# Optimization experiments

Measured on AMD Instinct MI355X. Metric: run time of the kernel, lower is better.

Reference implementation:

```python
import jax, jax.numpy as jnp
import numpy as np

B, N, M = 2, 16200, 128
DIM, QK_DIM, HEADS, GS = 256, 256, 8, 128


def setup_inputs() -> dict:
    key = jax.random.key(0)
    ks = jax.random.split(key, 10)
    sorted_x = jax.random.normal(ks[0], (B, N, DIM), dtype=jnp.float32)
    prototypes = jax.random.normal(ks[1], (B, M, DIM), dtype=jnp.float32)
    # idx_last must be a per-batch permutation of 0..N-1 (scatter-back to original order)
    idx_last = jnp.argsort(jax.random.uniform(ks[2], (B, N)), axis=-1).astype(jnp.int32)[..., None]
    s = 0.02
    Wq = jax.random.normal(ks[3], (DIM, QK_DIM), dtype=jnp.float32) * s
    Wk = jax.random.normal(ks[4], (DIM, QK_DIM), dtype=jnp.float32) * s
    Wv = jax.random.normal(ks[5], (DIM, DIM), dtype=jnp.float32) * s
    Wpk = jax.random.normal(ks[6], (DIM, QK_DIM), dtype=jnp.float32) * s
    Wpv = jax.random.normal(ks[7], (DIM, DIM), dtype=jnp.float32) * s
    Wproj = jax.random.normal(ks[8], (DIM, DIM), dtype=jnp.float32) * s
    return {"sorted_x": sorted_x, "idx_last": idx_last, "prototypes": prototypes,
            "Wq": Wq, "Wk": Wk, "Wv": Wv, "Wpk": Wpk, "Wpv": Wpv, "Wproj": Wproj}


def _iasa(sorted_x, idx_last, prototypes, Wq, Wk, Wv, Wpk, Wpv, Wproj):
    b, n, dim = sorted_x.shape
    h = HEADS
    gs = min(n, GS)
    ng = (n + gs - 1) // gs
    pad_n = ng * gs - n
    dq = Wq.shape[1] // h   # qk head dim
    dv = Wv.shape[1] // h   # v head dim
    scale = 1.0 / jnp.sqrt(jnp.asarray(dq, sorted_x.dtype))

    q = sorted_x @ Wq
    k = sorted_x @ Wk
    v = sorted_x @ Wv

    # pad q with flipped tail (pad_n tokens) -> [b, ng*gs, qk]
    q_pad = jnp.concatenate([q, q[:, n - pad_n:n][:, ::-1]], axis=1)
    qh = q_pad.reshape(b, ng, gs, h, dq).transpose(0, 1, 3, 2, 4)  # b ng h gs d

    def windows(t, c):
        # pad with flipped last (pad_n + gs) tokens -> length (ng+1)*gs, then
        # overlapping windows of 2*gs with stride gs (== torch unfold)
        t_pad = jnp.concatenate([t, t[:, n - pad_n - gs:n][:, ::-1]], axis=1)
        tr = t_pad.reshape(b, ng + 1, gs, c)
        win = jnp.concatenate([tr[:, :-1], tr[:, 1:]], axis=2)  # b ng 2gs c
        return win.reshape(b, ng, 2 * gs, h, c // h).transpose(0, 1, 3, 2, 4)  # b ng h 2gs d

    kw = windows(k, Wk.shape[1])
    vw = windows(v, Wv.shape[1])

    # local overlapping-window attention
    a1 = jax.nn.softmax(jnp.einsum('bghqd,bghkd->bghqk', qh, kw) * scale, axis=-1)
    o1 = jnp.einsum('bghqk,bghkd->bghqd', a1, vw)

    # global prototype cross-attention
    kg = (prototypes @ Wpk).reshape(b, -1, h, dq).transpose(0, 2, 1, 3)  # b h m d
    vg = (prototypes @ Wpv).reshape(b, -1, h, dv).transpose(0, 2, 1, 3)
    a2 = jax.nn.softmax(jnp.einsum('bghqd,bhmd->bghqm', qh, kg) * scale, axis=-1)
    o2 = jnp.einsum('bghqm,bhmd->bghqd', a2, vg)

    out = (o1 + o2).transpose(0, 1, 3, 2, 4).reshape(b, ng * gs, h * dv)[:, :n]

    # scatter back to original order: result[b, idx[b,i], c] = out[b, i, c]
    idx = jnp.broadcast_to(idx_last, out.shape)
    b_idx = jnp.arange(b)[:, None, None]
    c_idx = jnp.arange(out.shape[-1])[None, None, :]
    out = out.at[b_idx, idx, c_idx].set(out)
    return out @ Wproj


def reference(sorted_x, idx_last, prototypes, Wq, Wk, Wv, Wpk, Wpv, Wproj):
    return _iasa(sorted_x, idx_last, prototypes, Wq, Wk, Wv, Wpk, Wpv, Wproj)
```

## Files before the change

kernel.cpp:

```cpp
#include <hip/hip_runtime.h>


typedef unsigned short u16;
typedef unsigned int   u32;
typedef __attribute__((ext_vector_type(8))) u16   u16x8;
typedef __attribute__((ext_vector_type(4))) u16   u16x4;
typedef __attribute__((ext_vector_type(8))) short bf16x8;
typedef __attribute__((ext_vector_type(4))) float f32x4;

#define NB   2
#define NN   16200
#define MM   128
#define NH   8
#define NGRP 127
#define APAD 72

static __device__ __forceinline__ u16 f2bf(float f) {
  u32 u = __float_as_uint(f);
  return (u16)((u + 0x7FFFu + ((u >> 16) & 1u)) >> 16);
}

static __device__ __forceinline__ f32x4 mfma16(bf16x8 a, bf16x8 b, f32x4 c) {
  return __builtin_amdgcn_mfma_f32_16x16x32_bf16(a, b, c, 0, 0, 0);
}

__global__ void prep_wt(const float* __restrict__ w0, const float* __restrict__ w1,
                        const float* __restrict__ w2, const float* __restrict__ w3,
                        const float* __restrict__ w4, const float* __restrict__ w5,
                        u16* __restrict__ wt) {
  int m = blockIdx.y;
  const float* W = m == 0 ? w0 : m == 1 ? w1 : m == 2 ? w2 : m == 3 ? w3 : m == 4 ? w4 : w5;
  int t = blockIdx.x * 256 + threadIdx.x;
  int o = t >> 8, i = t & 255;
  wt[((size_t)(m * 256 + o) << 8) + i] = f2bf(W[(i << 8) + o]);
}

template <bool AF32, bool CF32>
__global__ __launch_bounds__(256) void gemm_bt(
    const void* __restrict__ Av, int numRows,
    const u16* __restrict__ Bt,
    void* __restrict__ Cv, int ldc,
    const int* __restrict__ idx)
{
  __shared__ __attribute__((aligned(16))) u16 sA[128 * APAD];
  __shared__ __attribute__((aligned(16))) u16 sB[128 * APAD];
  int rowBase = blockIdx.x << 7;
  int colBase = blockIdx.y << 7;
  int tid = threadIdx.x;
  int lane = tid & 63, w = tid >> 6;
  int wr = (w >> 1) << 6, wc = (w & 1) << 6;
  int lr = lane & 15, lg = lane >> 4;

  f32x4 acc[4][4];
#pragma unroll
  for (int i = 0; i < 4; ++i)
#pragma unroll
    for (int j = 0; j < 4; ++j) acc[i][j] = (f32x4)0.0f;

  for (int kt = 0; kt < 4; ++kt) {
#pragma unroll
    for (int i = 0; i < 4; ++i) {
      int e = tid + (i << 8);
      int r = e >> 3;
      int cc = (e & 7) << 3;
      int gr = rowBase + r;
      gr = gr < numRows ? gr : 0;
      if constexpr (AF32) {
        const float* A = (const float*)Av;
        f32x4 a0 = *(const f32x4*)(A + ((size_t)gr << 8) + (kt << 6) + cc);
        f32x4 a1 = *(const f32x4*)(A + ((size_t)gr << 8) + (kt << 6) + cc + 4);
        u16x8 val;
#pragma unroll
        for (int j = 0; j < 4; ++j) { val[j] = f2bf(a0[j]); val[4 + j] = f2bf(a1[j]); }
        *(u16x8*)(sA + r * APAD + cc) = val;
      } else {
        const u16* A = (const u16*)Av;
        *(u16x8*)(sA + r * APAD + cc) =
            *(const u16x8*)(A + ((size_t)gr << 8) + (kt << 6) + cc);
      }
      *(u16x8*)(sB + r * APAD + cc) =
          *(const u16x8*)(Bt + ((size_t)(colBase + r) << 8) + (kt << 6) + cc);
    }
    __syncthreads();
#pragma unroll
    for (int kk = 0; kk < 2; ++kk) {
      bf16x8 af[4], bfv[4];
#pragma unroll
      for (int m = 0; m < 4; ++m)
        af[m] = *(const bf16x8*)(sA + (wr + (m << 4) + lr) * APAD + (kk << 5) + (lg << 3));
#pragma unroll
      for (int n = 0; n < 4; ++n)
        bfv[n] = *(const bf16x8*)(sB + (wc + (n << 4) + lr) * APAD + (kk << 5) + (lg << 3));
#pragma unroll
      for (int m = 0; m < 4; ++m)
#pragma unroll
        for (int n = 0; n < 4; ++n) acc[m][n] = mfma16(af[m], bfv[n], acc[m][n]);
    }
    __syncthreads();
  }

#pragma unroll
  for (int m = 0; m < 4; ++m) {
    int row0 = rowBase + wr + (m << 4) + (lg << 2);
#pragma unroll
    for (int r = 0; r < 4; ++r) {
      int rr = row0 + r;
      if (rr >= numRows) continue;
      size_t orow = rr;
      if (idx) {
        int b = rr / NN;
        orow = (size_t)b * NN + idx[rr];
      }
#pragma unroll
      for (int n = 0; n < 4; ++n) {
        int col = colBase + wc + (n << 4) + lr;
        if constexpr (CF32) {
          ((float*)Cv)[orow * ldc + col] = acc[m][n][r];
        } else {
          ((u16*)Cv)[orow * ldc + col] = f2bf(acc[m][n][r]);
        }
      }
    }
  }
}

__global__ __launch_bounds__(256) void attn_kernel(
    const u16* __restrict__ qkv,
    const u16* __restrict__ kgvg,
    u16* __restrict__ outa)
{
  __shared__ __attribute__((aligned(16))) u16 sKV[256 * 40];
  __shared__ __attribute__((aligned(16))) u16 sVgt[32 * 136];
  __shared__ __attribute__((aligned(16))) u16 sP[4][16 * 264];

  int bid = blockIdx.x;
  int qh = bid & 1;
  int rest = bid >> 1;
  int g = rest % NGRP;
  int h = (rest / NGRP) & 7;
  int b = rest / (NGRP * NH);

  int tid = threadIdx.x, lane = tid & 63, w = tid >> 6;
  int lr = lane & 15, lg = lane >> 4;

  const size_t bOff = (size_t)b * NN * 768;
  const int hoff = h << 5;
  const int kbase = g << 7;

#pragma unroll
  for (int i = 0; i < 4; ++i) {
    int e = tid + (i << 8);
    int r = e >> 2, c = (e & 3) << 3;
    int kp = kbase + r;
    int tok = kp < NN ? kp : 2 * NN - 1 - kp;
    *(u16x8*)(sKV + r * 40 + c) =
        *(const u16x8*)(qkv + bOff + (size_t)tok * 768 + 256 + hoff + c);
  }
#pragma unroll
  for (int i = 0; i < 2; ++i) {
    int e = tid + (i << 8);
    int r = e >> 2, c = (e & 3) << 3;
    u16x8 v = *(const u16x8*)(kgvg + ((size_t)(b * MM + r) << 9) + 256 + hoff + c);
#pragma unroll
    for (int u = 0; u < 8; ++u) {
      int dv = c + u;
      sVgt[dv * 136 + (r ^ ((((dv >> 3) & 3)) << 3))] = v[u];
    }
  }
  __syncthreads();

  const float scale = 0.17677669529663687f;
  int qrow = (qh << 6) + (w << 4) + lr;
  int qtok = kbase + qrow;
  qtok = qtok < NN ? qtok : 2 * NN - 1 - qtok;
  bf16x8 qf = *(const bf16x8*)(qkv + bOff + (size_t)qtok * 768 + hoff + (lg << 3));

  f32x4 z = (f32x4)0.0f;
  f32x4 s[16];
#pragma unroll
  for (int kt = 0; kt < 16; ++kt) {
    bf16x8 kf = *(const bf16x8*)(sKV + ((kt << 4) + lr) * 40 + (lg << 3));
    s[kt] = mfma16(kf, qf, z);
  }
  float mx = -1e30f;
#pragma unroll
  for (int kt = 0; kt < 16; ++kt)
    mx = fmaxf(mx, fmaxf(fmaxf(s[kt][0], s[kt][1]), fmaxf(s[kt][2], s[kt][3])));
  mx = fmaxf(mx, __shfl_xor(mx, 16, 64));
  mx = fmaxf(mx, __shfl_xor(mx, 32, 64));
  float sum = 0.f;
#pragma unroll
  for (int kt = 0; kt < 16; ++kt)
#pragma unroll
    for (int r = 0; r < 4; ++r) {
      float p = __expf((s[kt][r] - mx) * scale);
      s[kt][r] = p;
      sum += p;
    }
  sum += __shfl_xor(sum, 16, 64);
  sum += __shfl_xor(sum, 32, 64);
  float inv = 1.0f / sum;
#pragma unroll
  for (int kt = 0; kt < 16; ++kt) {
    u16x4 pk;
#pragma unroll
    for (int r = 0; r < 4; ++r) pk[r] = f2bf(s[kt][r] * inv);
    *(u16x4*)(&sP[w][lr * 264 + (kt << 4) + (lg << 2)]) = pk;
  }
  __syncthreads();

#pragma unroll
  for (int i = 0; i < 4; ++i) {
    int e = tid + (i << 8);
    int r = e >> 2, c = (e & 3) << 3;
    int kp = kbase + r;
    int tok = kp < NN ? kp : 2 * NN - 1 - kp;
    u16x8 v = *(const u16x8*)(qkv + bOff + (size_t)tok * 768 + 512 + hoff + c);
#pragma unroll
    for (int u = 0; u < 8; ++u) {
      int dv = c + u;
      sKV[dv * 264 + (r ^ ((((dv >> 3) & 3)) << 3))] = v[u];
    }
  }
  __syncthreads();

  const int sw0 = ((lr >> 3) & 3) << 3;
  const int sw1 = (((16 + lr) >> 3) & 3) << 3;

  f32x4 o0 = z, o1 = z;
#pragma unroll
  for (int kb = 0; kb < 8; ++kb) {
    int k0 = (kb << 5) + (lg << 3);
    bf16x8 pf = *(const bf16x8*)(&sP[w][lr * 264 + k0]);
    bf16x8 v0 = *(const bf16x8*)(sKV + lr * 264 + (k0 ^ sw0));
    bf16x8 v1 = *(const bf16x8*)(sKV + (16 + lr) * 264 + (k0 ^ sw1));
    o0 = mfma16(v0, pf, o0);
    o1 = mfma16(v1, pf, o1);
  }

  f32x4 sg[8];
#pragma unroll
  for (int kt = 0; kt < 8; ++kt) {
    bf16x8 kf = *(const bf16x8*)(kgvg + ((size_t)(b * MM + (kt << 4) + lr) << 9) + hoff + (lg << 3));
    sg[kt] = mfma16(kf, qf, z);
  }
  float mx2 = -1e30f;
#pragma unroll
  for (int kt = 0; kt < 8; ++kt)
    mx2 = fmaxf(mx2, fmaxf(fmaxf(sg[kt][0], sg[kt][1]), fmaxf(sg[kt][2], sg[kt][3])));
  mx2 = fmaxf(mx2, __shfl_xor(mx2, 16, 64));
  mx2 = fmaxf(mx2, __shfl_xor(mx2, 32, 64));
  float sum2 = 0.f;
#pragma unroll
  for (int kt = 0; kt < 8; ++kt)
#pragma unroll
    for (int r = 0; r < 4; ++r) {
      float p = __expf((sg[kt][r] - mx2) * scale);
      sg[kt][r] = p;
      sum2 += p;
    }
  sum2 += __shfl_xor(sum2, 16, 64);
  sum2 += __shfl_xor(sum2, 32, 64);
  float inv2 = 1.0f / sum2;
#pragma unroll
  for (int kt = 0; kt < 8; ++kt) {
    u16x4 pk;
#pragma unroll
    for (int r = 0; r < 4; ++r) pk[r] = f2bf(sg[kt][r] * inv2);
    *(u16x4*)(&sP[w][lr * 264 + (kt << 4) + (lg << 2)]) = pk;
  }
#pragma unroll
  for (int kb = 0; kb < 4; ++kb) {
    int k0 = (kb << 5) + (lg << 3);
    bf16x8 pf = *(const bf16x8*)(&sP[w][lr * 264 + k0]);
    bf16x8 v0 = *(const bf16x8*)(sVgt + lr * 136 + (k0 ^ sw0));
    bf16x8 v1 = *(const bf16x8*)(sVgt + (16 + lr) * 136 + (k0 ^ sw1));
    o0 = mfma16(v0, pf, o0);
    o1 = mfma16(v1, pf, o1);
  }

  int token = kbase + (qh << 6) + (w << 4) + lr;
  if (token < NN) {
    size_t base = ((size_t)b * NN + token) * 256 + hoff;
    u16x4 w0v, w1v;
#pragma unroll
    for (int r = 0; r < 4; ++r) {
      w0v[r] = f2bf(o0[r]);
      w1v[r] = f2bf(o1[r]);
    }
    *(u16x4*)(outa + base + (lg << 2)) = w0v;
    *(u16x4*)(outa + base + 16 + (lg << 2)) = w1v;
  }
}

extern "C" void kernel_launch(void* const* d_in, const int* in_sizes, int n_in,
                              void* d_out, int out_size, void* d_ws, size_t ws_size,
                              hipStream_t stream) {
  const float* x     = (const float*)d_in[0];
  const int*   idx   = (const int*)d_in[1];
  const float* proto = (const float*)d_in[2];
  const float* Wq    = (const float*)d_in[3];
  const float* Wk    = (const float*)d_in[4];
  const float* Wv    = (const float*)d_in[5];
  const float* Wpk   = (const float*)d_in[6];
  const float* Wpv   = (const float*)d_in[7];
  const float* Wproj = (const float*)d_in[8];

  u16* wt   = (u16*)d_ws;
  u16* qkv  = wt + (size_t)1536 * 256;
  u16* kgvg = qkv + (size_t)32400 * 768;
  u16* attn = kgvg + (size_t)256 * 512;

  prep_wt<<<dim3(256, 6), 256, 0, stream>>>(Wq, Wk, Wv, Wpk, Wpv, Wproj, wt);
  gemm_bt<true, false><<<dim3(254, 6), 256, 0, stream>>>(x, NB * NN, wt, qkv, 768, nullptr);
  gemm_bt<true, false><<<dim3(2, 4), 256, 0, stream>>>(proto, NB * MM, wt + (size_t)768 * 256,
                                                       kgvg, 512, nullptr);
  attn_kernel<<<dim3(NB * NH * NGRP * 2), 256, 0, stream>>>(qkv, kgvg, attn);
  gemm_bt<false, true><<<dim3(254, 2), 256, 0, stream>>>(attn, NB * NN, wt + (size_t)1280 * 256,
                                                         d_out, 256, idx);
}
```

Baseline: 222.7 us.

## Prefetch V into registers early, load prototype V directly, split softmax reductions

The attention kernel now issues the global loads for the window's V tile alongside the K tile, keeps them in registers, and writes them transposed into shared memory after the softmax. This hides V load latency behind the QK and softmax work. The prototype V shared buffer and its transpose are removed, and each lane gathers its bf16 MFMA operands straight from global memory with scalar loads. The max and sum reductions use four independent accumulators to shorten dependency chains, and bf16 conversion switches to the HIP intrinsic. In exchange, register pressure rises and the global gathers are uncoalesced 2-byte reads.

Measured after the change: 225.9 us. Within noise of the previous version (+1.5%).

```diff
diff --git a/kernel.cpp b/kernel.cpp
--- a/kernel.cpp
+++ b/kernel.cpp
@@ -1,4 +1,5 @@
 #include <hip/hip_runtime.h>
+#include <hip/hip_bf16.h>
 
 
 typedef unsigned short u16;
@@ -18,6 +19,13 @@
 static __device__ __forceinline__ u16 f2bf(float f) {
   u32 u = __float_as_uint(f);
   return (u16)((u + 0x7FFFu + ((u >> 16) & 1u)) >> 16);
+}
+
+static __device__ __forceinline__ u16 f2bfn(float f) {
+  __hip_bfloat16 h = __float2bfloat16(f);
+  u16 r;
+  __builtin_memcpy(&r, &h, 2);
+  return r;
 }
 
 static __device__ __forceinline__ f32x4 mfma16(bf16x8 a, bf16x8 b, f32x4 c) {
@@ -130,7 +138,6 @@
     u16* __restrict__ outa)
 {
   __shared__ __attribute__((aligned(16))) u16 sKV[256 * 40];
-  __shared__ __attribute__((aligned(16))) u16 sVgt[32 * 136];
   __shared__ __attribute__((aligned(16))) u16 sP[4][16 * 264];
 
   int bid = blockIdx.x;
@@ -147,6 +154,8 @@
   const int hoff = h << 5;
   const int kbase = g << 7;
 
+  u16x8 vreg[4];
+  int vr_[4], vc_[4];
 #pragma unroll
   for (int i = 0; i < 4; ++i) {
     int e = tid + (i << 8);
@@ -155,17 +164,8 @@
     int tok = kp < NN ? kp : 2 * NN - 1 - kp;
     *(u16x8*)(sKV + r * 40 + c) =
         *(const u16x8*)(qkv + bOff + (size_t)tok * 768 + 256 + hoff + c);
-  }
-#pragma unroll
-  for (int i = 0; i < 2; ++i) {
-    int e = tid + (i << 8);
-    int r = e >> 2, c = (e & 3) << 3;
-    u16x8 v = *(const u16x8*)(kgvg + ((size_t)(b * MM + r) << 9) + 256 + hoff + c);
-#pragma unroll
-    for (int u = 0; u < 8; ++u) {
-      int dv = c + u;
-      sVgt[dv * 136 + (r ^ ((((dv >> 3) & 3)) << 3))] = v[u];
-    }
+    vreg[i] = *(const u16x8*)(qkv + bOff + (size_t)tok * 768 + 512 + hoff + c);
+    vr_[i] = r; vc_[i] = c;
   }
   __syncthreads();
 
@@ -182,21 +182,26 @@
     bf16x8 kf = *(const bf16x8*)(sKV + ((kt << 4) + lr) * 40 + (lg << 3));
     s[kt] = mfma16(kf, qf, z);
   }
-  float mx = -1e30f;
-#pragma unroll
-  for (int kt = 0; kt < 16; ++kt)
-    mx = fmaxf(mx, fmaxf(fmaxf(s[kt][0], s[kt][1]), fmaxf(s[kt][2], s[kt][3])));
+  float m0 = -1e30f, m1 = -1e30f, m2 = -1e30f, m3 = -1e30f;
+#pragma unroll
+  for (int kt = 0; kt < 16; ++kt) {
+    m0 = fmaxf(m0, s[kt][0]); m1 = fmaxf(m1, s[kt][1]);
+    m2 = fmaxf(m2, s[kt][2]); m3 = fmaxf(m3, s[kt][3]);
+  }
+  float mx = fmaxf(fmaxf(m0, m1), fmaxf(m2, m3));
   mx = fmaxf(mx, __shfl_xor(mx, 16, 64));
   mx = fmaxf(mx, __shfl_xor(mx, 32, 64));
-  float sum = 0.f;
-#pragma unroll
-  for (int kt = 0; kt < 16; ++kt)
-#pragma unroll
-    for (int r = 0; r < 4; ++r) {
-      float p = __expf((s[kt][r] - mx) * scale);
-      s[kt][r] = p;
-      sum += p;
-    }
+  float u0 = 0.f, u1 = 0.f, u2 = 0.f, u3 = 0.f;
+#pragma unroll
+  for (int kt = 0; kt < 16; ++kt) {
+    float p0 = __expf((s[kt][0] - mx) * scale);
+    float p1 = __expf((s[kt][1] - mx) * scale);
+    float p2 = __expf((s[kt][2] - mx) * scale);
+    float p3 = __expf((s[kt][3] - mx) * scale);
+    s[kt][0] = p0; s[kt][1] = p1; s[kt][2] = p2; s[kt][3] = p3;
+    u0 += p0; u1 += p1; u2 += p2; u3 += p3;
+  }
+  float sum = (u0 + u1) + (u2 + u3);
   sum += __shfl_xor(sum, 16, 64);
   sum += __shfl_xor(sum, 32, 64);
   float inv = 1.0f / sum;
@@ -204,22 +209,18 @@
   for (int kt = 0; kt < 16; ++kt) {
     u16x4 pk;
 #pragma unroll
-    for (int r = 0; r < 4; ++r) pk[r] = f2bf(s[kt][r] * inv);
+    for (int r = 0; r < 4; ++r) pk[r] = f2bfn(s[kt][r] * inv);
     *(u16x4*)(&sP[w][lr * 264 + (kt << 4) + (lg << 2)]) = pk;
   }
   __syncthreads();
 
 #pragma unroll
   for (int i = 0; i < 4; ++i) {
-    int e = tid + (i << 8);
-    int r = e >> 2, c = (e & 3) << 3;
-    int kp = kbase + r;
-    int tok = kp < NN ? kp : 2 * NN - 1 - kp;
-    u16x8 v = *(const u16x8*)(qkv + bOff + (size_t)tok * 768 + 512 + hoff + c);
+    int r = vr_[i], c = vc_[i];
 #pragma unroll
     for (int u = 0; u < 8; ++u) {
       int dv = c + u;
-      sKV[dv * 264 + (r ^ ((((dv >> 3) & 3)) << 3))] = v[u];
+      sKV[dv * 264 + (r ^ ((((dv >> 3) & 3)) << 3))] = vreg[i][u];
     }
   }
   __syncthreads();
@@ -244,21 +245,36 @@
     bf16x8 kf = *(const bf16x8*)(kgvg + ((size_t)(b * MM + (kt << 4) + lr) << 9) + hoff + (lg << 3));
     sg[kt] = mfma16(kf, qf, z);
   }
-  float mx2 = -1e30f;
-#pragma unroll
-  for (int kt = 0; kt < 8; ++kt)
-    mx2 = fmaxf(mx2, fmaxf(fmaxf(sg[kt][0], sg[kt][1]), fmaxf(sg[kt][2], sg[kt][3])));
+  bf16x8 vg0[4], vg1[4];
+#pragma unroll
+  for (int kb = 0; kb < 4; ++kb) {
+#pragma unroll
+    for (int j = 0; j < 8; ++j) {
+      size_t row = ((size_t)(b * MM + (kb << 5) + (lg << 3) + j) << 9) + 256 + hoff;
+      vg0[kb][j] = (short)kgvg[row + lr];
+      vg1[kb][j] = (short)kgvg[row + 16 + lr];
+    }
+  }
+  float n0 = -1e30f, n1 = -1e30f, n2 = -1e30f, n3 = -1e30f;
+#pragma unroll
+  for (int kt = 0; kt < 8; ++kt) {
+    n0 = fmaxf(n0, sg[kt][0]); n1 = fmaxf(n1, sg[kt][1]);
+    n2 = fmaxf(n2, sg[kt][2]); n3 = fmaxf(n3, sg[kt][3]);
+  }
+  float mx2 = fmaxf(fmaxf(n0, n1), fmaxf(n2, n3));
   mx2 = fmaxf(mx2, __shfl_xor(mx2, 16, 64));
   mx2 = fmaxf(mx2, __shfl_xor(mx2, 32, 64));
-  float sum2 = 0.f;
-#pragma unroll
-  for (int kt = 0; kt < 8; ++kt)
-#pragma unroll
-    for (int r = 0; r < 4; ++r) {
-      float p = __expf((sg[kt][r] - mx2) * scale);
-      sg[kt][r] = p;
-      sum2 += p;
-    }
+  float t0 = 0.f, t1 = 0.f, t2 = 0.f, t3 = 0.f;
+#pragma unroll
+  for (int kt = 0; kt < 8; ++kt) {
+    float p0 = __expf((sg[kt][0] - mx2) * scale);
+    float p1 = __expf((sg[kt][1] - mx2) * scale);
+    float p2 = __expf((sg[kt][2] - mx2) * scale);
+    float p3 = __expf((sg[kt][3] - mx2) * scale);
+    sg[kt][0] = p0; sg[kt][1] = p1; sg[kt][2] = p2; sg[kt][3] = p3;
+    t0 += p0; t1 += p1; t2 += p2; t3 += p3;
+  }
+  float sum2 = (t0 + t1) + (t2 + t3);
   sum2 += __shfl_xor(sum2, 16, 64);
   sum2 += __shfl_xor(sum2, 32, 64);
   float inv2 = 1.0f / sum2;
@@ -266,17 +282,15 @@
   for (int kt = 0; kt < 8; ++kt) {
     u16x4 pk;
 #pragma unroll
-    for (int r = 0; r < 4; ++r) pk[r] = f2bf(sg[kt][r] * inv2);
+    for (int r = 0; r < 4; ++r) pk[r] = f2bfn(sg[kt][r] * inv2);
     *(u16x4*)(&sP[w][lr * 264 + (kt << 4) + (lg << 2)]) = pk;
   }
 #pragma unroll
   for (int kb = 0; kb < 4; ++kb) {
     int k0 = (kb << 5) + (lg << 3);
     bf16x8 pf = *(const bf16x8*)(&sP[w][lr * 264 + k0]);
-    bf16x8 v0 = *(const bf16x8*)(sVgt + lr * 136 + (k0 ^ sw0));
-    bf16x8 v1 = *(const bf16x8*)(sVgt + (16 + lr) * 136 + (k0 ^ sw1));
-    o0 = mfma16(v0, pf, o0);
-    o1 = mfma16(v1, pf, o1);
+    o0 = mfma16(vg0[kb], pf, o0);
+    o1 = mfma16(vg1[kb], pf, o1);
   }
 
   int token = kbase + (qh << 6) + (w << 4) + lr;
@@ -285,8 +299,8 @@
     u16x4 w0v, w1v;
 #pragma unroll
     for (int r = 0; r < 4; ++r) {
-      w0v[r] = f2bf(o0[r]);
-      w1v[r] = f2bf(o1[r]);
+      w0v[r] = f2bfn(o0[r]);
+      w1v[r] = f2bfn(o1[r]);
     }
     *(u16x4*)(outa + base + (lg << 2)) = w0v;
     *(u16x4*)(outa + base + 16 + (lg << 2)) = w1v;
```
